# Performance work log

Hardware: AMD Instinct MI355X
Metric: run time of the kernel (lower is better)

The kernel has to match this reference:

```python
import jax, jax.numpy as jnp
import numpy as np

B, S, HID = 4, 2048, 2048
NH, NKV, D = 16, 8, 128
RK, RV = 16, 16
HPG = NH // NKV
SCALING = D ** -0.5
NEG = -1e9


def _rope(x, cos, sin):
    # x: [B, S, H, D]; cos/sin: [S, D//2]. Gemma split-half complex rotation.
    x1, x2 = jnp.split(x, 2, axis=-1)
    c = cos[None, :, None, :]
    s = sin[None, :, None, :]
    return jnp.concatenate([x1 * c - x2 * s, x1 * s + x2 * c], axis=-1)


def setup_inputs() -> dict:
    key = jax.random.key(0)
    ks = jax.random.split(key, 8)
    hidden_states = jax.random.normal(ks[0], (B, S, HID), dtype=jnp.float32)
    # RoPE frequencies (theta=10000)
    inv_freq = 1.0 / (10000.0 ** (np.arange(0, D, 2, dtype=np.float32) / D))
    ang = np.arange(S, dtype=np.float32)[:, None] * inv_freq[None, :]
    freqs_cos = jnp.asarray(np.cos(ang), dtype=jnp.float32)
    freqs_sin = jnp.asarray(np.sin(ang), dtype=jnp.float32)
    kv_write_indices = jnp.arange(S, dtype=jnp.int32)
    # causal additive mask [1,1,S,S]
    causal = jnp.tril(jnp.ones((S, S), dtype=bool))
    mask = jnp.where(causal, 0.0, NEG).astype(jnp.float32)[None, None]
    sc = 0.02
    W_q = jax.random.normal(ks[1], (NH * D, HID), dtype=jnp.float32) * sc
    W_k = jax.random.normal(ks[2], (NKV * D, HID), dtype=jnp.float32) * sc
    W_v = jax.random.normal(ks[3], (NKV * D, HID), dtype=jnp.float32) * sc
    o_proj_w = jax.random.normal(ks[4], (HID, NH * D), dtype=jnp.float32) * sc
    V_r_basis = jax.random.normal(ks[5], (NH, D, RK), dtype=jnp.float32) * (D ** -0.5)
    Z_v_basis = jax.random.normal(ks[6], (NKV, D, RV), dtype=jnp.float32) * (D ** -0.5)
    return {"hidden_states": hidden_states, "freqs_cos": freqs_cos, "freqs_sin": freqs_sin,
            "kv_write_indices": kv_write_indices, "mask": mask, "W_q": W_q, "W_k": W_k,
            "W_v": W_v, "o_proj_w": o_proj_w, "V_r_basis": V_r_basis, "Z_v_basis": Z_v_basis}


def reference(hidden_states, freqs_cos, freqs_sin, kv_write_indices, mask,
              W_q, W_k, W_v, o_proj_w, V_r_basis, Z_v_basis):
    bsz, q_len, _ = hidden_states.shape
    q = (hidden_states @ W_q.T).reshape(bsz, q_len, NH, D)
    k = (hidden_states @ W_k.T).reshape(bsz, q_len, NKV, D)
    v = (hidden_states @ W_v.T).reshape(bsz, q_len, NKV, D)

    # project K per-head onto its group's basis (vectorized over the head loop)
    head_to_group = jnp.arange(NH) // HPG                       # [NH]
    k_per_head = k[:, :, head_to_group, :]                      # [B,S,NH,D]
    pk = jnp.einsum('bshd,hdr->bshr', k_per_head, V_r_basis)    # [B,S,NH,RK]
    pv = jnp.einsum('bqgd,gdr->bqgr', v, Z_v_basis)             # [B,S,NKV,RV]

    # factorized cache write (scatter along seq dim), prefill: kv_seq_len = S
    kv_seq_len = q_len
    cache_pk = jnp.zeros((bsz, kv_seq_len, NH, RK), hidden_states.dtype)
    cache_pv = jnp.zeros((bsz, kv_seq_len, NKV, RV), hidden_states.dtype)
    cache_pk = cache_pk.at[:, kv_write_indices].set(pk)
    cache_pv = cache_pv.at[:, kv_write_indices].set(pv)

    # reconstruct K/V from compressed cache
    k_hat = jnp.einsum('bshr,hrd->bshd', cache_pk, jnp.swapaxes(V_r_basis, -1, -2))
    v_hat = jnp.einsum('bsgr,grd->bsgd', cache_pv, jnp.swapaxes(Z_v_basis, -1, -2))

    # RoPE post-reconstruction
    q_rot = _rope(q, freqs_cos[:q_len], freqs_sin[:q_len])
    k_rot = _rope(k_hat, freqs_cos[:kv_seq_len], freqs_sin[:kv_seq_len])

    # GQA: repeat kv heads
    v_g = jnp.repeat(v_hat, HPG, axis=2)                        # [B,S,NH,D]

    scores = jnp.einsum('bqhd,bkhd->bhqk', q_rot, k_rot) * SCALING
    scores = scores + mask[:, :, :q_len, :kv_seq_len]
    probs = jax.nn.softmax(scores.astype(jnp.float32), axis=-1).astype(hidden_states.dtype)
    out = jnp.einsum('bhqk,bkhd->bqhd', probs, v_g)
    out = out.reshape(bsz, q_len, NH * D)
    return out @ o_proj_w.T
```

## Files before the change

### kernel.cpp

```cpp
#include <hip/hip_runtime.h>

typedef unsigned short ushort8 __attribute__((ext_vector_type(8)));
typedef short s16x8 __attribute__((ext_vector_type(8)));
typedef float f32x4 __attribute__((ext_vector_type(4)));

#define AS1 __attribute__((address_space(1)))
#define AS3 __attribute__((address_space(3)))

#define B_    4
#define S_    2048
#define HID_  2048
#define NH_   16
#define NKV_  8
#define D_    128
#define RK_   16
#define SCALING_ 0.08838834764831845f
#define LOG2E_   1.4426950408889634f
#define NEGBIG   -1.0e30f

__device__ __forceinline__ float bf2f(unsigned short u) {
  union { unsigned int i; float f; } x; x.i = ((unsigned int)u) << 16; return x.f;
}
__device__ __forceinline__ unsigned short f2bf(float f) {
  union { float f; unsigned int i; } x; x.f = f;
  unsigned int r = x.i + 0x7fffu + ((x.i >> 16) & 1u);
  return (unsigned short)(r >> 16);
}

__global__ __launch_bounds__(256) void cvt_bf16(const float* __restrict__ in,
                                                unsigned short* __restrict__ out,
                                                int n8) {
  int i = blockIdx.x * 256 + threadIdx.x;
  const int stride = gridDim.x * 256;
  for (; i < n8; i += stride) {
    const float4 a = ((const float4*)in)[i * 2];
    const float4 b = ((const float4*)in)[i * 2 + 1];
    ushort8 u;
    u[0] = f2bf(a.x); u[1] = f2bf(a.y); u[2] = f2bf(a.z); u[3] = f2bf(a.w);
    u[4] = f2bf(b.x); u[5] = f2bf(b.y); u[6] = f2bf(b.z); u[7] = f2bf(b.w);
    *(ushort8*)&out[i * 8] = u;
  }
}

__global__ __launch_bounds__(256) void wfuse(const float* __restrict__ W_k,
                                             const float* __restrict__ W_v,
                                             const float* __restrict__ Vr,
                                             const float* __restrict__ Zv,
                                             unsigned short* __restrict__ Wf) {
  const int idx = blockIdx.x;
  const int cc = blockIdx.y * 256;
  const int tid = threadIdx.x;
  const bool isK = idx < 16;
  const int hg = isK ? idx : (idx - 16);
  const int wrow0 = isK ? (idx * 16) : (256 + (idx - 16) * 16);
  const float* W = isK ? &W_k[(size_t)((hg >> 1) * 128) * HID_]
                       : &W_v[(size_t)(hg * 128) * HID_];
  const float* P = isK ? &Vr[(size_t)hg * 128 * 16] : &Zv[(size_t)hg * 128 * 16];
  __shared__ float Wl[32][257];
  float acc[16] = {};
  for (int d0 = 0; d0 < 128; d0 += 32) {
    __syncthreads();
#pragma unroll 8
    for (int dd = 0; dd < 32; ++dd)
      Wl[dd][tid] = W[(size_t)(d0 + dd) * HID_ + cc + tid];
    __syncthreads();
#pragma unroll 8
    for (int dd = 0; dd < 32; ++dd) {
      const float w = Wl[dd][tid];
#pragma unroll
      for (int r = 0; r < 16; ++r) acc[r] += w * P[(d0 + dd) * 16 + r];
    }
  }
#pragma unroll
  for (int r = 0; r < 16; ++r)
    Wf[(size_t)(wrow0 + r) * HID_ + cc + tid] = f2bf(acc[r]);
}

template<bool CBF>
__global__ __launch_bounds__(256) void gemm_mfma(const unsigned short* __restrict__ A,
                                                 const unsigned short* __restrict__ Bb,
                                                 void* __restrict__ C_,
                                                 int M, int N, int K) {
  __shared__ unsigned short Ash[128 * 64];
  __shared__ unsigned short Bsh[128 * 64];
  const int tid = threadIdx.x;
  const int w = tid >> 6, l = tid & 63, lg = l >> 4, ll = l & 15;
  const int wr = w >> 1, wc = w & 1;
  const int flat = blockIdx.y * gridDim.x + blockIdx.x;
  const int cpx = (gridDim.x * gridDim.y) >> 3;
  const int swz = (flat & 7) * cpx + (flat >> 3);
  const int bm = (swz / gridDim.x) * 128, bn = (swz % gridDim.x) * 128;

  f32x4 acc[4][4];
#pragma unroll
  for (int i = 0; i < 4; i++)
#pragma unroll
    for (int j = 0; j < 4; j++) acc[i][j] = (f32x4){0.f, 0.f, 0.f, 0.f};

  const int srow = tid >> 3;
  const int sslot = tid & 7;

  for (int k0 = 0; k0 < K; k0 += 64) {
    __syncthreads();
#pragma unroll
    for (int c = 0; c < 4; ++c) {
      const int row = c * 32 + srow;
      const int ss = sslot ^ (row & 7);
      const unsigned short* srcA = &A[(size_t)(bm + row) * K + k0 + ss * 8];
      const unsigned short* srcB = &Bb[(size_t)(bn + row) * K + k0 + ss * 8];
      char* dstA = ((char*)Ash) + c * 4096 + w * 1024;
      char* dstB = ((char*)Bsh) + c * 4096 + w * 1024;
      __builtin_amdgcn_global_load_lds((const AS1 void*)srcA, (AS3 void*)dstA, 16, 0, 0);
      __builtin_amdgcn_global_load_lds((const AS1 void*)srcB, (AS3 void*)dstB, 16, 0, 0);
    }
    __syncthreads();

#pragma unroll
    for (int ks = 0; ks < 2; ++ks) {
      s16x8 af[4], bf_[4];
#pragma unroll
      for (int mi = 0; mi < 4; ++mi) {
        const int row = wr * 64 + mi * 16 + ll;
        af[mi] = *(const s16x8*)&Ash[row * 64 + (((ks * 4 + lg) ^ (row & 7)) * 8)];
      }
#pragma unroll
      for (int ni = 0; ni < 4; ++ni) {
        const int row = wc * 64 + ni * 16 + ll;
        bf_[ni] = *(const s16x8*)&Bsh[row * 64 + (((ks * 4 + lg) ^ (row & 7)) * 8)];
      }
#pragma unroll
      for (int mi = 0; mi < 4; ++mi)
#pragma unroll
        for (int ni = 0; ni < 4; ++ni)
          acc[mi][ni] = __builtin_amdgcn_mfma_f32_16x16x32_bf16(af[mi], bf_[ni], acc[mi][ni], 0, 0, 0);
    }
  }

#pragma unroll
  for (int mi = 0; mi < 4; ++mi)
#pragma unroll
    for (int ni = 0; ni < 4; ++ni)
#pragma unroll
      for (int j = 0; j < 4; ++j) {
        const int row = bm + wr * 64 + mi * 16 + lg * 4 + j;
        const int col = bn + wc * 64 + ni * 16 + ll;
        if (CBF) ((unsigned short*)C_)[(size_t)row * N + col] = f2bf(acc[mi][ni][j]);
        else     ((float*)C_)[(size_t)row * N + col] = acc[mi][ni][j];
      }
}

__global__ __launch_bounds__(256) void rope_q(unsigned short* __restrict__ q,
                                              const float* __restrict__ cosT,
                                              const float* __restrict__ sinT) {
  const int p = blockIdx.x * 256 + threadIdx.x;
  const int d = p & 63;
  const int h = (p >> 6) & 15;
  const int s = (p >> 10) & 2047;
  const int b = p >> 21;
  const size_t base = (((size_t)b * S_ + s) * NH_ + h) * D_ + d;
  const float x1 = bf2f(q[base]), x2 = bf2f(q[base + 64]);
  const float c = cosT[s * 64 + d], sn = sinT[s * 64 + d];
  const float sc = SCALING_ * LOG2E_;
  q[base]      = f2bf((x1 * c - x2 * sn) * sc);
  q[base + 64] = f2bf((x1 * sn + x2 * c) * sc);
}

__global__ __launch_bounds__(256) void expand_k(const float* __restrict__ pkpv,
                                                const float* __restrict__ Vr,
                                                const float* __restrict__ cosT,
                                                const float* __restrict__ sinT,
                                                unsigned short* __restrict__ kr) {
  const int s0 = blockIdx.x * 32, h = blockIdx.y, b = blockIdx.z;
  const int tid = threadIdx.x;
  __shared__ float pkS[32][17];
  if (tid < 128) {
    const int r_ = tid >> 2, c4 = (tid & 3) * 4;
    float4 v = *(const float4*)&pkpv[(size_t)(b * S_ + s0 + r_) * 384 + h * 16 + c4];
    pkS[r_][c4 + 0] = v.x; pkS[r_][c4 + 1] = v.y;
    pkS[r_][c4 + 2] = v.z; pkS[r_][c4 + 3] = v.w;
  }
  __syncthreads();
  const int row = tid >> 3, dl = tid & 7;
  float kh[16];
#pragma unroll
  for (int j = 0; j < 16; j++) {
    const int d = dl + 8 * j;
    const float4* w = (const float4*)&Vr[((size_t)h * D_ + d) * RK_];
    float a = 0.f;
#pragma unroll
    for (int q4 = 0; q4 < 4; q4++) {
      float4 wv = w[q4];
      a += pkS[row][q4 * 4 + 0] * wv.x + pkS[row][q4 * 4 + 1] * wv.y
         + pkS[row][q4 * 4 + 2] * wv.z + pkS[row][q4 * 4 + 3] * wv.w;
    }
    kh[j] = a;
  }
  const int pos = s0 + row;
  const size_t o = (((size_t)b * NH_ + h) * S_ + pos) * D_;
#pragma unroll
  for (int j = 0; j < 8; j++) {
    const int d = dl + 8 * j;
    const float c = cosT[pos * 64 + d], sn = sinT[pos * 64 + d];
    kr[o + d]      = f2bf(kh[j] * c - kh[j + 8] * sn);
    kr[o + d + 64] = f2bf(kh[j] * sn + kh[j + 8] * c);
  }
}

__global__ __launch_bounds__(256) void expand_v(const float* __restrict__ pkpv,
                                                const float* __restrict__ Zv,
                                                unsigned short* __restrict__ vh) {
  const int s0 = blockIdx.x * 32, g = blockIdx.y, b = blockIdx.z;
  const int tid = threadIdx.x;
  __shared__ float pvS[32][17];
  if (tid < 128) {
    const int r_ = tid >> 2, c4 = (tid & 3) * 4;
    float4 v = *(const float4*)&pkpv[(size_t)(b * S_ + s0 + r_) * 384 + 256 + g * 16 + c4];
    pvS[r_][c4 + 0] = v.x; pvS[r_][c4 + 1] = v.y;
    pvS[r_][c4 + 2] = v.z; pvS[r_][c4 + 3] = v.w;
  }
  __syncthreads();
  const int row = tid >> 3, dl = tid & 7;
  const size_t o = (((size_t)b * NKV_ + g) * S_ + s0 + row) * D_;
#pragma unroll
  for (int j = 0; j < 16; j++) {
    const int d = dl + 8 * j;
    const float4* w = (const float4*)&Zv[((size_t)g * D_ + d) * RK_];
    float a = 0.f;
#pragma unroll
    for (int q4 = 0; q4 < 4; q4++) {
      float4 wv = w[q4];
      a += pvS[row][q4 * 4 + 0] * wv.x + pvS[row][q4 * 4 + 1] * wv.y
         + pvS[row][q4 * 4 + 2] * wv.z + pvS[row][q4 * 4 + 3] * wv.w;
    }
    vh[o + d] = f2bf(a);
  }
}

template<bool SPLIT>
__global__ __launch_bounds__(256) void attn_mfma(const unsigned short* __restrict__ q,
                                                 const unsigned short* __restrict__ kr,
                                                 const unsigned short* __restrict__ vh,
                                                 unsigned short* __restrict__ outp,
                                                 unsigned short* __restrict__ P0,
                                                 unsigned short* __restrict__ P1,
                                                 float2* __restrict__ ml0,
                                                 float2* __restrict__ ml1) {
  int qt, h, b, half;
  if constexpr (SPLIT) {
    const int flat = ((int)blockIdx.z * 16 + (int)blockIdx.y) * 32 + (int)blockIdx.x;
    const int swz = (flat & 7) * 256 + (flat >> 3);
    qt = 15 - (swz & 15);
    half = (swz >> 4) & 1;
    h = (swz >> 5) & 15;
    b = swz >> 9;
  } else {
    const int flat = ((int)blockIdx.z * 16 + (int)blockIdx.y) * 16 + (int)blockIdx.x;
    const int swz = (flat & 7) * 128 + (flat >> 3);
    qt = 15 - (swz & 15);
    half = 0;
    h = (swz >> 4) & 15;
    b = swz >> 8;
  }
  const int g = h >> 1;
  const int tid = threadIdx.x;
  const int w = tid >> 6, l = tid & 63, lg = l >> 4, ll = l & 15;

  __shared__ unsigned short Klds[2][64 * 128];
  __shared__ unsigned short Vt[2][128 * 64];
  __shared__ unsigned short Ps[4][32 * 64];

  const int qr0 = qt * 128 + w * 32;
  const int kt0   = SPLIT ? (half ? qt + 1 : 0)          : 0;
  const int ktend = SPLIT ? (half ? 2 * qt + 1 : qt)     : 2 * qt + 1;
  const int kmy = 2 * qt + (w >> 1);

  s16x8 qf[2][4];
#pragma unroll
  for (int mi = 0; mi < 2; ++mi)
#pragma unroll
    for (int ks = 0; ks < 4; ++ks)
      qf[mi][ks] = *(const s16x8*)&q[(((size_t)b * S_ + qr0 + mi * 16 + ll) * NH_ + h) * D_ + ks * 32 + lg * 8];

  f32x4 o[2][8];
#pragma unroll
  for (int mi = 0; mi < 2; ++mi)
#pragma unroll
    for (int nd = 0; nd < 8; ++nd) o[mi][nd] = (f32x4){0.f, 0.f, 0.f, 0.f};
  float m_[2][4], l_[2][4];
#pragma unroll
  for (int mi = 0; mi < 2; ++mi)
#pragma unroll
    for (int j = 0; j < 4; ++j) { m_[mi][j] = NEGBIG; l_[mi][j] = 0.f; }

  const unsigned short* kbase = &kr[(((size_t)b * NH_ + h) * S_) * D_];
  const unsigned short* vbase = &vh[(((size_t)b * NKV_ + g) * S_) * D_];
  const int vk = (tid & 31) * 2, d0v = (tid >> 5) * 16;

  ushort8 va0, va1, vb0, vb1;
  {
    const unsigned short* kb0 = kbase + (size_t)kt0 * 64 * D_;
#pragma unroll
    for (int c = 0; c < 4; ++c) {
      const int ro = c * 16 + w * 4 + lg;
      const int ss = ll ^ (ro & 7);
      const unsigned short* src = kb0 + ro * D_ + ss * 8;
      char* dst = ((char*)&Klds[0][0]) + c * 4096 + w * 1024;
      __builtin_amdgcn_global_load_lds((const AS1 void*)src, (AS3 void*)dst, 16, 0, 0);
    }
    const unsigned short* v0 = vbase + (size_t)(kt0 * 64 + vk) * D_ + d0v;
    va0 = *(const ushort8*)v0; va1 = *(const ushort8*)(v0 + 8);
    vb0 = *(const ushort8*)(v0 + D_); vb1 = *(const ushort8*)(v0 + D_ + 8);
#pragma unroll
    for (int j = 0; j < 8; ++j) {
      const int d1 = d0v + j, d2 = d0v + 8 + j;
      *(unsigned int*)&Vt[0][d1 * 64 + (((vk >> 3) ^ (d1 & 7)) * 8) + (vk & 7)] =
          (unsigned int)va0[j] | ((unsigned int)vb0[j] << 16);
      *(unsigned int*)&Vt[0][d2 * 64 + (((vk >> 3) ^ (d2 & 7)) * 8) + (vk & 7)] =
          (unsigned int)va1[j] | ((unsigned int)vb1[j] << 16);
    }
  }
  __syncthreads();

  for (int kt = kt0; kt <= ktend; ++kt) {
    const int p = (kt - kt0) & 1;
    if (kt < ktend) {
      const unsigned short* kb2 = kbase + (size_t)(kt + 1) * 64 * D_;
#pragma unroll
      for (int c = 0; c < 4; ++c) {
        const int ro = c * 16 + w * 4 + lg;
        const int ss = ll ^ (ro & 7);
        const unsigned short* src = kb2 + ro * D_ + ss * 8;
        char* dst = ((char*)&Klds[p ^ 1][0]) + c * 4096 + w * 1024;
        __builtin_amdgcn_global_load_lds((const AS1 void*)src, (AS3 void*)dst, 16, 0, 0);
      }
      const unsigned short* v0 = vbase + (size_t)((kt + 1) * 64 + vk) * D_ + d0v;
      va0 = *(const ushort8*)v0; va1 = *(const ushort8*)(v0 + 8);
      vb0 = *(const ushort8*)(v0 + D_); vb1 = *(const ushort8*)(v0 + D_ + 8);
    }

    if (kt <= kmy) {
      f32x4 s[2][4];
#pragma unroll
      for (int mi = 0; mi < 2; ++mi)
#pragma unroll
        for (int ni = 0; ni < 4; ++ni) s[mi][ni] = (f32x4){0.f, 0.f, 0.f, 0.f};
#pragma unroll
      for (int ks = 0; ks < 4; ++ks) {
#pragma unroll
        for (int ni = 0; ni < 4; ++ni) {
          const int row = ni * 16 + ll;
          const s16x8 kf = *(const s16x8*)&Klds[p][row * 128 + (((ks * 4 + lg) ^ (row & 7)) * 8)];
          s[0][ni] = __builtin_amdgcn_mfma_f32_16x16x32_bf16(qf[0][ks], kf, s[0][ni], 0, 0, 0);
          s[1][ni] = __builtin_amdgcn_mfma_f32_16x16x32_bf16(qf[1][ks], kf, s[1][ni], 0, 0, 0);
        }
      }

      const bool diag = (kt == kmy);
      float lm[2][4];
#pragma unroll
      for (int mi = 0; mi < 2; ++mi)
#pragma unroll
        for (int j = 0; j < 4; ++j) {
          if (diag) {
            const int qg = qr0 + mi * 16 + lg * 4 + j;
#pragma unroll
            for (int ni = 0; ni < 4; ++ni)
              if (kt * 64 + ni * 16 + ll > qg) s[mi][ni][j] = NEGBIG;
          }
          lm[mi][j] = fmaxf(fmaxf(s[mi][0][j], s[mi][1][j]),
                            fmaxf(s[mi][2][j], s[mi][3][j]));
        }
      float excess = lm[0][0] - m_[0][0];
#pragma unroll
      for (int mi = 0; mi < 2; ++mi)
#pragma unroll
        for (int j = 0; j < 4; ++j) excess = fmaxf(excess, lm[mi][j] - m_[mi][j]);
      const bool slow = __any(excess > 11.5f);

#pragma unroll
      for (int mi = 0; mi < 2; ++mi)
#pragma unroll
        for (int j = 0; j < 4; ++j) {
          float ps_[4];
          if (slow) {
            float mt = lm[mi][j];
            mt = fmaxf(mt, __shfl_xor(mt, 1));
            mt = fmaxf(mt, __shfl_xor(mt, 2));
            mt = fmaxf(mt, __shfl_xor(mt, 4));
            mt = fmaxf(mt, __shfl_xor(mt, 8));
            const float mnew = fmaxf(m_[mi][j], mt);
            const float al = exp2f(m_[mi][j] - mnew);
            m_[mi][j] = mnew;
            float sum = 0.f;
#pragma unroll
            for (int ni = 0; ni < 4; ++ni) { ps_[ni] = exp2f(s[mi][ni][j] - mnew); sum += ps_[ni]; }
            l_[mi][j] = l_[mi][j] * al + sum;
#pragma unroll
            for (int nd = 0; nd < 8; ++nd) o[mi][nd][j] *= al;
          } else {
            float sum = 0.f;
#pragma unroll
            for (int ni = 0; ni < 4; ++ni) { ps_[ni] = exp2f(s[mi][ni][j] - m_[mi][j]); sum += ps_[ni]; }
            l_[mi][j] += sum;
          }
          const int prow = mi * 16 + lg * 4 + j;
#pragma unroll
          for (int nq = 0; nq < 2; ++nq) {
            unsigned int u;
            asm("v_cvt_pk_bf16_f32 %0, %1, %2" : "=v"(u) : "v"(ps_[nq * 2]), "v"(ps_[nq * 2 + 1]));
            const int c0 = nq * 32 + ll, c1 = nq * 32 + 16 + ll;
            Ps[w][prow * 64 + (((c0 >> 3) ^ (prow & 7)) * 8) + (ll & 7)] = (unsigned short)u;
            Ps[w][prow * 64 + (((c1 >> 3) ^ (prow & 7)) * 8) + (ll & 7)] = (unsigned short)(u >> 16);
          }
        }

      s16x8 pa[2][2];
#pragma unroll
      for (int mi = 0; mi < 2; ++mi)
#pragma unroll
        for (int ks2 = 0; ks2 < 2; ++ks2) {
          const int prow = mi * 16 + ll;
          pa[mi][ks2] = *(const s16x8*)&Ps[w][prow * 64 + (((ks2 * 4 + lg) ^ (prow & 7)) * 8)];
        }
#pragma unroll
      for (int nd = 0; nd < 8; ++nd) {
#pragma unroll
        for (int ks2 = 0; ks2 < 2; ++ks2) {
          const int vr = nd * 16 + ll;
          const s16x8 vbf = *(const s16x8*)&Vt[p][vr * 64 + (((ks2 * 4 + lg) ^ (vr & 7)) * 8)];
          o[0][nd] = __builtin_amdgcn_mfma_f32_16x16x32_bf16(pa[0][ks2], vbf, o[0][nd], 0, 0, 0);
          o[1][nd] = __builtin_amdgcn_mfma_f32_16x16x32_bf16(pa[1][ks2], vbf, o[1][nd], 0, 0, 0);
        }
      }
    }

    if (kt < ktend) {
#pragma unroll
      for (int j = 0; j < 8; ++j) {
        const int d1 = d0v + j, d2 = d0v + 8 + j;
        *(unsigned int*)&Vt[p ^ 1][d1 * 64 + (((vk >> 3) ^ (d1 & 7)) * 8) + (vk & 7)] =
            (unsigned int)va0[j] | ((unsigned int)vb0[j] << 16);
        *(unsigned int*)&Vt[p ^ 1][d2 * 64 + (((vk >> 3) ^ (d2 & 7)) * 8) + (vk & 7)] =
            (unsigned int)va1[j] | ((unsigned int)vb1[j] << 16);
      }
    }
    __syncthreads();
  }

#pragma unroll
  for (int mi = 0; mi < 2; ++mi)
#pragma unroll
    for (int j = 0; j < 4; ++j) {
      float ls = l_[mi][j];
      ls += __shfl_xor(ls, 1);
      ls += __shfl_xor(ls, 2);
      ls += __shfl_xor(ls, 4);
      ls += __shfl_xor(ls, 8);
      if constexpr (SPLIT) {
        unsigned short* Ph = half ? P1 : P0;
        float2* mlh = half ? ml1 : ml0;
        const size_t ridx = ((size_t)b * NH_ + h) * S_ + qr0 + mi * 16 + lg * 4 + j;
        unsigned short* op = &Ph[ridx * D_ + ll];
#pragma unroll
        for (int nd = 0; nd < 8; ++nd) op[nd * 16] = f2bf(o[mi][nd][j]);
        if (ll == 0) mlh[ridx] = make_float2(m_[mi][j], ls);
      } else {
        const float inv = 1.f / ls;
        const size_t rowg = (size_t)b * S_ + qr0 + mi * 16 + lg * 4 + j;
        unsigned short* op = &outp[rowg * (NH_ * D_) + h * D_ + ll];
#pragma unroll
        for (int nd = 0; nd < 8; ++nd) op[nd * 16] = f2bf(o[mi][nd][j] * inv);
      }
    }
}

__global__ __launch_bounds__(256) void attn_combine(const unsigned short* __restrict__ P0,
                                                    const unsigned short* __restrict__ P1,
                                                    const float2* __restrict__ ml0,
                                                    const float2* __restrict__ ml1,
                                                    unsigned short* __restrict__ outp) {
  const int s = blockIdx.x, b = blockIdx.y;
  const int tid = threadIdx.x;
  const int h = tid >> 4, d0 = (tid & 15) * 8;
  const size_t ridx = ((size_t)b * NH_ + h) * S_ + s;
  const float2 a = ml0[ridx], c = ml1[ridx];
  const float m = fmaxf(a.x, c.x);
  const float a0 = exp2f(a.x - m), a1 = exp2f(c.x - m);
  const float inv = 1.f / (a0 * a.y + a1 * c.y);
  const ushort8 u0 = *(const ushort8*)&P0[ridx * D_ + d0];
  const ushort8 u1 = *(const ushort8*)&P1[ridx * D_ + d0];
  ushort8 r;
#pragma unroll
  for (int j = 0; j < 8; ++j)
    r[j] = f2bf((a0 * bf2f(u0[j]) + a1 * bf2f(u1[j])) * inv);
  *(ushort8*)&outp[((size_t)b * S_ + s) * (NH_ * D_) + h * D_ + d0] = r;
}

extern "C" void kernel_launch(void* const* d_in, const int* in_sizes, int n_in,
                              void* d_out, int out_size, void* d_ws, size_t ws_size,
                              hipStream_t stream) {
  const float* hidden = (const float*)d_in[0];
  const float* cosT   = (const float*)d_in[1];
  const float* sinT   = (const float*)d_in[2];
  const float* W_q    = (const float*)d_in[5];
  const float* W_k    = (const float*)d_in[6];
  const float* W_v    = (const float*)d_in[7];
  const float* W_o    = (const float*)d_in[8];
  const float* Vr     = (const float*)d_in[9];
  const float* Zv     = (const float*)d_in[10];
  float* out = (float*)d_out;

  char* ws = (char*)d_ws;
  unsigned short* hb     = (unsigned short*)(ws + 0);
  unsigned short* attn_b = (unsigned short*)(ws + 0);
  unsigned short* P0     = (unsigned short*)(ws + 0);
  unsigned short* q_b    = (unsigned short*)(ws + 33554432);
  unsigned short* kr_b   = (unsigned short*)(ws + 67108864);
  unsigned short* Wf     = (unsigned short*)(ws + 100663296);
  unsigned short* vh_b   = (unsigned short*)(ws + 100663296);
  unsigned short* WR1    = (unsigned short*)(ws + 117440512);
  float*          pkpv   = (float*)(ws + 117440512);
  unsigned short* P1     = (unsigned short*)(ws + 130023424);
  float2*         ml0    = (float2*)(ws + 163577856);
  float2*         ml1    = (float2*)(ws + 164626432);
  const size_t NEED_SPLIT = 165675008ull;
  const bool split = (ws_size >= NEED_SPLIT);

  const int M = B_ * S_;

  cvt_bf16<<<2048, 256, 0, stream>>>(hidden, hb, (B_ * S_ * HID_) / 8);
  cvt_bf16<<<2048, 256, 0, stream>>>(W_q, WR1, (HID_ * HID_) / 8);
  gemm_mfma<true><<<dim3(16, 64), 256, 0, stream>>>(hb, WR1, q_b, M, 2048, HID_);

  wfuse<<<dim3(24, 8), 256, 0, stream>>>(W_k, W_v, Vr, Zv, Wf);
  gemm_mfma<false><<<dim3(3, 64), 256, 0, stream>>>(hb, Wf, pkpv, M, 384, HID_);

  rope_q<<<(B_ * S_ * NH_ * 64) / 256, 256, 0, stream>>>(q_b, cosT, sinT);

  expand_k<<<dim3(S_ / 32, NH_, B_), 256, 0, stream>>>(pkpv, Vr, cosT, sinT, kr_b);
  expand_v<<<dim3(S_ / 32, NKV_, B_), 256, 0, stream>>>(pkpv, Zv, vh_b);

  cvt_bf16<<<2048, 256, 0, stream>>>(W_o, WR1, (HID_ * HID_) / 8);

  if (split) {
    attn_mfma<true><<<dim3(32, 16, 4), 256, 0, stream>>>(q_b, kr_b, vh_b, nullptr,
                                                         P0, P1, ml0, ml1);
    attn_combine<<<dim3(S_, B_), 256, 0, stream>>>(P0, P1, ml0, ml1, q_b);
    gemm_mfma<false><<<dim3(16, 64), 256, 0, stream>>>(q_b, WR1, out, M, HID_, HID_);
  } else {
    attn_mfma<false><<<dim3(16, 16, 4), 256, 0, stream>>>(q_b, kr_b, vh_b, attn_b,
                                                          nullptr, nullptr, nullptr, nullptr);
    gemm_mfma<false><<<dim3(16, 64), 256, 0, stream>>>(attn_b, WR1, out, M, HID_, HID_);
  }
}
```

Before: 747.0 us.

## Use 256x256-tile 8-wave phased GEMM for Q and output projections

Adds a new GEMM kernel with 256x256 output tiles, 512 threads, double-buffered direct global-to-LDS loads with XOR swizzle, and a four-phase schedule that interleaves prefetch of the next K tile with MFMA work using explicit waitcnt, barriers and priority hints. It replaces the 128x128 GEMM for the Q projection and the output projection, aiming for more data reuse per tile and better overlap of memory and compute. Larger tiles give only 256 blocks on a large GPU, which may leave some compute units idle or unbalanced, and they use much more LDS and registers per block.

```diff
diff --git a/kernel.cpp b/kernel.cpp
--- a/kernel.cpp
+++ b/kernel.cpp
@@ -149,6 +149,116 @@
       }
 }
 
+template<bool CBF>
+__global__ __launch_bounds__(512) void gemm256_8ph(const unsigned short* __restrict__ A,
+                                                   const unsigned short* __restrict__ Bb,
+                                                   void* __restrict__ C_,
+                                                   int M, int N, int K) {
+  __shared__ unsigned short Lds[2][2][256 * 64];
+  const int tid = threadIdx.x;
+  const int w = tid >> 6, l = tid & 63, lg = l >> 4, ll = l & 15;
+  const int wr = w >> 2;
+  const int wc = w & 3;
+  const int flat = blockIdx.y * gridDim.x + blockIdx.x;
+  const int cpx = (gridDim.x * gridDim.y) >> 3;
+  const int swz = (flat & 7) * cpx + (flat >> 3);
+  const int bm = (swz / gridDim.x) * 256, bn = (swz % gridDim.x) * 256;
+
+  f32x4 acc[8][4];
+#pragma unroll
+  for (int i = 0; i < 8; i++)
+#pragma unroll
+    for (int j = 0; j < 4; j++) acc[i][j] = (f32x4){0.f, 0.f, 0.f, 0.f};
+
+  auto stage = [&](int op, int hh, int slot, int kk) {
+    const unsigned short* base = (op == 0) ? A : Bb;
+    const int r0 = (op == 0) ? bm : bn;
+#pragma unroll
+    for (int i = 0; i < 2; ++i) {
+      const int r = hh * 128 + i * 64 + (tid >> 3);
+      const int ss = (tid & 7) ^ (r & 7);
+      const unsigned short* src = &base[(size_t)(r0 + r) * K + kk + ss * 8];
+      unsigned short* dstb = &Lds[slot][op][(hh * 128 + i * 64 + (w << 3)) * 64];
+      __builtin_amdgcn_global_load_lds((const AS1 void*)src, (AS3 void*)dstb, 16, 0, 0);
+    }
+  };
+
+  const int NT = K >> 6;
+
+  stage(0, 0, 0, 0);
+  stage(1, 0, 0, 0);
+  stage(1, 1, 0, 0);
+  stage(0, 1, 0, 0);
+
+#define GPHASE(MIH, NIH, WAITN, DO_PF)                                          \
+  {                                                                             \
+    if (WAITN == 4)      asm volatile("s_waitcnt vmcnt(4)" ::: "memory");       \
+    else if (WAITN == 6) asm volatile("s_waitcnt vmcnt(6)" ::: "memory");       \
+    __builtin_amdgcn_sched_barrier(0);                                          \
+    __builtin_amdgcn_s_barrier();                                               \
+    __builtin_amdgcn_sched_barrier(0);                                          \
+    s16x8 af[4][2], bf_[2][2];                                                  \
+    _Pragma("unroll")                                                           \
+    for (int mi2 = 0; mi2 < 4; ++mi2)                                           \
+      _Pragma("unroll")                                                         \
+      for (int ks = 0; ks < 2; ++ks) {                                          \
+        const int row = (MIH) * 128 + wr * 64 + mi2 * 16 + ll;                  \
+        af[mi2][ks] = *(const s16x8*)&Lds[s][0][row * 64 +                      \
+                          (((ks * 4 + lg) ^ (row & 7)) * 8)];                   \
+      }                                                                         \
+    _Pragma("unroll")                                                           \
+    for (int ni2 = 0; ni2 < 2; ++ni2)                                           \
+      _Pragma("unroll")                                                         \
+      for (int ks = 0; ks < 2; ++ks) {                                          \
+        const int row = (NIH) * 128 + wc * 32 + ni2 * 16 + ll;                  \
+        bf_[ni2][ks] = *(const s16x8*)&Lds[s][1][row * 64 +                     \
+                          (((ks * 4 + lg) ^ (row & 7)) * 8)];                   \
+      }                                                                         \
+    __builtin_amdgcn_s_setprio(1);                                              \
+    _Pragma("unroll")                                                           \
+    for (int mi2 = 0; mi2 < 4; ++mi2)                                           \
+      _Pragma("unroll")                                                         \
+      for (int ni2 = 0; ni2 < 2; ++ni2)                                         \
+        _Pragma("unroll")                                                       \
+        for (int ks = 0; ks < 2; ++ks)                                          \
+          acc[(MIH) * 4 + mi2][(NIH) * 2 + ni2] =                               \
+              __builtin_amdgcn_mfma_f32_16x16x32_bf16(                          \
+                  af[mi2][ks], bf_[ni2][ks],                                    \
+                  acc[(MIH) * 4 + mi2][(NIH) * 2 + ni2], 0, 0, 0);              \
+    __builtin_amdgcn_s_setprio(0);                                              \
+    DO_PF                                                                       \
+  }
+
+  for (int t = 0; t < NT; ++t) {
+    const int s = t & 1;
+    const int s2 = s ^ 1;
+    const bool hn = (t + 1 < NT);
+    const int k1 = (t + 1) << 6;
+    GPHASE(0, 0, 4, { if (hn) { stage(0, 0, s2, k1); stage(1, 0, s2, k1); } })
+    GPHASE(0, 1, 6, { if (hn) { stage(1, 1, s2, k1); } })
+    GPHASE(1, 1, 6, { if (hn) { stage(0, 1, s2, k1); } })
+    GPHASE(1, 0, 0, {})
+  }
+#undef GPHASE
+
+#pragma unroll
+  for (int mih = 0; mih < 2; ++mih)
+#pragma unroll
+    for (int mi2 = 0; mi2 < 4; ++mi2)
+#pragma unroll
+      for (int nih = 0; nih < 2; ++nih)
+#pragma unroll
+        for (int ni2 = 0; ni2 < 2; ++ni2)
+#pragma unroll
+          for (int j = 0; j < 4; ++j) {
+            const int row = bm + mih * 128 + wr * 64 + mi2 * 16 + lg * 4 + j;
+            const int col = bn + nih * 128 + wc * 32 + ni2 * 16 + ll;
+            const float v = acc[mih * 4 + mi2][nih * 2 + ni2][j];
+            if (CBF) ((unsigned short*)C_)[(size_t)row * N + col] = f2bf(v);
+            else     ((float*)C_)[(size_t)row * N + col] = v;
+          }
+}
+
 __global__ __launch_bounds__(256) void rope_q(unsigned short* __restrict__ q,
                                               const float* __restrict__ cosT,
                                               const float* __restrict__ sinT) {
@@ -530,7 +640,7 @@
 
   cvt_bf16<<<2048, 256, 0, stream>>>(hidden, hb, (B_ * S_ * HID_) / 8);
   cvt_bf16<<<2048, 256, 0, stream>>>(W_q, WR1, (HID_ * HID_) / 8);
-  gemm_mfma<true><<<dim3(16, 64), 256, 0, stream>>>(hb, WR1, q_b, M, 2048, HID_);
+  gemm256_8ph<true><<<dim3(8, 32), 512, 0, stream>>>(hb, WR1, q_b, M, 2048, HID_);
 
   wfuse<<<dim3(24, 8), 256, 0, stream>>>(W_k, W_v, Vr, Zv, Wf);
   gemm_mfma<false><<<dim3(3, 64), 256, 0, stream>>>(hb, Wf, pkpv, M, 384, HID_);
@@ -546,10 +656,10 @@
     attn_mfma<true><<<dim3(32, 16, 4), 256, 0, stream>>>(q_b, kr_b, vh_b, nullptr,
                                                          P0, P1, ml0, ml1);
     attn_combine<<<dim3(S_, B_), 256, 0, stream>>>(P0, P1, ml0, ml1, q_b);
-    gemm_mfma<false><<<dim3(16, 64), 256, 0, stream>>>(q_b, WR1, out, M, HID_, HID_);
+    gemm256_8ph<false><<<dim3(8, 32), 512, 0, stream>>>(q_b, WR1, out, M, HID_, HID_);
   } else {
     attn_mfma<false><<<dim3(16, 16, 4), 256, 0, stream>>>(q_b, kr_b, vh_b, attn_b,
                                                           nullptr, nullptr, nullptr, nullptr);
-    gemm_mfma<false><<<dim3(16, 64), 256, 0, stream>>>(attn_b, WR1, out, M, HID_, HID_);
-  }
-}
+    gemm256_8ph<false><<<dim3(8, 32), 512, 0, stream>>>(attn_b, WR1, out, M, HID_, HID_);
+  }
+}
```

Result: faster. 708.0 us, median of 2 (-5.2%).
